# Kernel optimization log

Hardware: AMD Instinct MI355X
Metric: run time of the kernel (lower is better)

Reference implementation:

```python
import jax, jax.numpy as jnp
import numpy as np

N_NODES = 100000
N_EDGES = 1600000
D_FEAT = 128
HIDDEN = 128
N_CLASSES = 10
N_GRAPHS = 512


def setup_inputs() -> dict:
    key = jax.random.key(0)
    ks = jax.random.split(key, 8)
    x = jax.random.normal(ks[0], (N_NODES, D_FEAT), dtype=jnp.float32)
    edge_index = jax.random.randint(ks[1], (2, N_EDGES), 0, N_NODES, dtype=jnp.int64)
    batch = jnp.sort(jax.random.randint(ks[2], (N_NODES,), 0, N_GRAPHS, dtype=jnp.int64))
    s = 1.0 / np.sqrt(D_FEAT)
    W1 = jax.random.normal(ks[3], (D_FEAT, HIDDEN), dtype=jnp.float32) * s
    W2 = jax.random.normal(ks[4], (HIDDEN, HIDDEN), dtype=jnp.float32) * s
    W3 = jax.random.normal(ks[5], (HIDDEN, HIDDEN), dtype=jnp.float32) * s
    Wl = jax.random.normal(ks[6], (HIDDEN, N_CLASSES), dtype=jnp.float32) * s
    return {
        'x': x, 'edge_index': edge_index, 'batch': batch,
        'W1': W1, 'b1': jnp.zeros((HIDDEN,), jnp.float32),
        'W2': W2, 'b2': jnp.zeros((HIDDEN,), jnp.float32),
        'W3': W3, 'b3': jnp.zeros((HIDDEN,), jnp.float32),
        'Wl': Wl, 'bl': jnp.zeros((N_CLASSES,), jnp.float32),
    }


def _gcn_norm(edge_index, n_nodes):
    # add self-loops + symmetric normalization (PyG GCNConv defaults)
    loop = jnp.arange(n_nodes, dtype=edge_index.dtype)
    src = jnp.concatenate([edge_index[0], loop])
    dst = jnp.concatenate([edge_index[1], loop])
    deg = jax.ops.segment_sum(jnp.ones_like(dst, jnp.float32), dst, num_segments=n_nodes)
    dinv = jnp.where(deg > 0, jax.lax.rsqrt(deg), 0.0)
    norm = dinv[src] * dinv[dst]  # [E+N]
    return src, dst, norm


def _gcn_conv(x, src, dst, norm, W, b, n_nodes):
    h = x @ W                                   # [N, H]
    msg = norm[:, None] * h[src]                # gather + scale, [E+N, H]
    out = jax.ops.segment_sum(msg, dst, num_segments=n_nodes)  # scatter-add
    return out + b


def reference(x, edge_index, batch, W1, b1, W2, b2, W3, b3, Wl, bl):
    n = x.shape[0]
    src, dst, norm = _gcn_norm(edge_index, n)
    h = jax.nn.relu(_gcn_conv(x, src, dst, norm, W1, b1, n))
    h = jax.nn.relu(_gcn_conv(h, src, dst, norm, W2, b2, n))
    h = _gcn_conv(h, src, dst, norm, W3, b3, n)
    # global mean pool over graphs
    sums = jax.ops.segment_sum(h, batch, num_segments=N_GRAPHS)        # [G, H]
    cnts = jax.ops.segment_sum(jnp.ones((n,), jnp.float32), batch, num_segments=N_GRAPHS)
    pooled = sums / jnp.maximum(cnts, 1.0)[:, None]
    # dropout is identity in eval mode
    return pooled @ Wl + bl                                            # [G, C]
```

## Files before the change

### kernel.cpp

```cpp
#include <hip/hip_runtime.h>
#include <cstdint>
#include <cstddef>

typedef _Float16 half8 __attribute__((ext_vector_type(8)));
typedef float    f32x4 __attribute__((ext_vector_type(4)));

#define NBLK 512
#define BSHIFT 8

static __device__ __forceinline__ float4 ld4(const float* p) {
    return *reinterpret_cast<const float4*>(p);
}

static __device__ __forceinline__ void ld8h(const _Float16* p, float* f) {
    half8 v = *reinterpret_cast<const half8*>(p);
#pragma unroll
    for (int k = 0; k < 8; ++k) f[k] = (float)v[k];
}


__global__ __launch_bounds__(256)
void binA_count(const int* __restrict__ dst, int* __restrict__ cntM,
                int e, int nb, int tile) {
    __shared__ int lc[512];
    const int t = threadIdx.x, j = blockIdx.x;
    lc[t] = 0; lc[t + 256] = 0;
    __syncthreads();
    const int lo = j * tile;
    const int hi = min(e, lo + tile);
    for (int i = lo + t; i < hi; i += 256) atomicAdd(&lc[dst[i] >> BSHIFT], 1);
    __syncthreads();
    for (int b = t; b < nb; b += 256) cntM[b * NBLK + j] = lc[b];
}

__global__ __launch_bounds__(256)
void scan1_kernel(const int* __restrict__ cnt, int* __restrict__ blockSums, int n) {
    __shared__ int ts[256];
    const int t = threadIdx.x;
    const int base = blockIdx.x * 1024 + t * 4;
    int s = 0;
    if (base + 3 < n) {
        int4 q = *reinterpret_cast<const int4*>(cnt + base);
        s = q.x + q.y + q.z + q.w;
    } else {
#pragma unroll
        for (int j = 0; j < 4; ++j) if (base + j < n) s += cnt[base + j];
    }
    ts[t] = s;
    __syncthreads();
    for (int off = 128; off > 0; off >>= 1) {
        if (t < off) ts[t] += ts[t + off];
        __syncthreads();
    }
    if (t == 0) blockSums[blockIdx.x] = ts[0];
}

__global__ __launch_bounds__(1024)
void scan_top_kernel(const int* __restrict__ blockSums, int* __restrict__ blockOff,
                     int* __restrict__ total, int nb) {
    __shared__ int ls[1024];
    const int t = threadIdx.x;
    ls[t] = (t < nb) ? blockSums[t] : 0;
    __syncthreads();
    for (int off = 1; off < 1024; off <<= 1) {
        int v = (t >= off) ? ls[t - off] : 0;
        __syncthreads();
        ls[t] += v;
        __syncthreads();
    }
    if (t < nb) blockOff[t] = (t == 0) ? 0 : ls[t - 1];
    if (t == 1023) total[0] = ls[1023];
}

__global__ __launch_bounds__(256)
void scan2_kernel(const int* __restrict__ cnt, const int* __restrict__ blockOff,
                  int* __restrict__ outp, int n) {
    __shared__ int ts[256];
    const int t = threadIdx.x;
    const int base = blockIdx.x * 1024 + t * 4;
    int v[4] = {0, 0, 0, 0};
    if (base + 3 < n) {
        int4 q = *reinterpret_cast<const int4*>(cnt + base);
        v[0] = q.x; v[1] = q.y; v[2] = q.z; v[3] = q.w;
    } else {
#pragma unroll
        for (int j = 0; j < 4; ++j) if (base + j < n) v[j] = cnt[base + j];
    }
    int s = v[0] + v[1] + v[2] + v[3];
    ts[t] = s;
    __syncthreads();
    for (int off = 1; off < 256; off <<= 1) {
        int x = (t >= off) ? ts[t - off] : 0;
        __syncthreads();
        ts[t] += x;
        __syncthreads();
    }
    int excl = blockOff[blockIdx.x] + ((t == 0) ? 0 : ts[t - 1]);
#pragma unroll
    for (int j = 0; j < 4; ++j) {
        if (base + j < n) outp[base + j] = excl;
        excl += v[j];
    }
}

__global__ __launch_bounds__(256)
void binA_place(const int* __restrict__ src, const int* __restrict__ dst,
                const int* __restrict__ offM, int2* __restrict__ staging,
                int e, int nb, int tile) {
    __shared__ int cur[512];
    const int t = threadIdx.x, j = blockIdx.x;
    for (int b = t; b < nb; b += 256) cur[b] = offM[b * NBLK + j];
    __syncthreads();
    const int lo = j * tile;
    const int hi = min(e, lo + tile);
    for (int i = lo + t; i < hi; i += 256) {
        int s = src[i];
        int d = dst[i];
        int pos = atomicAdd(&cur[d >> BSHIFT], 1);
        staging[pos] = make_int2(s, d);
    }
}

__global__ __launch_bounds__(256)
void bucket_rows(const int2* __restrict__ staging, const int* __restrict__ offM,
                 int* __restrict__ rowptr, float* __restrict__ dinv,
                 int n, int nb, int e) {
    __shared__ int lc[256];
    __shared__ int ls[256];
    const int b = blockIdx.x, t = threadIdx.x;
    const int base = offM[b * NBLK];
    const int end  = (b + 1 < nb) ? offM[(b + 1) * NBLK] : e;
    const int d0 = b << BSHIFT;
    const int R  = min(n - d0, 256);
    lc[t] = 0;
    __syncthreads();
    for (int i = base + t; i < end; i += 256) atomicAdd(&lc[staging[i].y - d0], 1);
    __syncthreads();
    const int deg = lc[t];
    ls[t] = deg;
    __syncthreads();
    for (int off = 1; off < 256; off <<= 1) {
        int v = (t >= off) ? ls[t - off] : 0;
        __syncthreads();
        ls[t] += v;
        __syncthreads();
    }
    int excl = (t == 0) ? 0 : ls[t - 1];
    if (t < R) {
        rowptr[d0 + t] = base + excl;
        dinv[d0 + t]   = rsqrtf((float)(deg + 1));
    }
    if (b == nb - 1 && t == 0) rowptr[n] = e;
}

__global__ __launch_bounds__(256)
void bucket_scatter(const int2* __restrict__ staging, const int* __restrict__ offM,
                    const int* __restrict__ rowptr, const float* __restrict__ dinv,
                    int2* __restrict__ rec, int n, int nb, int e) {
    __shared__ int   cur[256];
    __shared__ float ldv[256];
    const int b = blockIdx.x, t = threadIdx.x;
    const int base = offM[b * NBLK];
    const int end  = (b + 1 < nb) ? offM[(b + 1) * NBLK] : e;
    const int d0 = b << BSHIFT;
    const int R  = min(n - d0, 256);
    if (t < R) {
        cur[t] = rowptr[d0 + t];
        ldv[t] = dinv[d0 + t];
    }
    __syncthreads();
    for (int i = base + t; i < end; i += 256) {
        int2 q = staging[i];
        int dl = q.y - d0;
        int pos = atomicAdd(&cur[dl], 1);
        float w = dinv[q.x] * ldv[dl];
        rec[pos] = make_int2(q.x, __float_as_int(w));
    }
}

template<int IN32>
__global__ __launch_bounds__(256)
void gemm_mfma_kernel(const void* __restrict__ Xv, const float* __restrict__ W,
                      _Float16* __restrict__ H16, int n) {
    __shared__ _Float16 Wt[128][136];
    __shared__ _Float16 Sw[4][16][136];

    const int t = threadIdx.x;
#pragma unroll
    for (int j = 0; j < 16; ++j) {
        int i4 = t + 256 * j;
        int k  = i4 >> 5;
        int c4 = (i4 & 31) * 4;
        float4 v = ld4(W + (size_t)i4 * 4);
        Wt[c4 + 0][k] = (_Float16)v.x;
        Wt[c4 + 1][k] = (_Float16)v.y;
        Wt[c4 + 2][k] = (_Float16)v.z;
        Wt[c4 + 3][k] = (_Float16)v.w;
    }
    __syncthreads();

    const int wave = t >> 6;
    const int l    = t & 63;
    const int lr   = l & 15;
    const int lk   = l >> 4;
    const int rowA = blockIdx.x * 64 + wave * 16 + lr;

    half8 a[4];
#pragma unroll
    for (int ks = 0; ks < 4; ++ks) {
#pragma unroll
        for (int j = 0; j < 8; ++j) a[ks][j] = (_Float16)0.f;
    }
    if (rowA < n) {
        if (IN32) {
            const float* X = (const float*)Xv;
#pragma unroll
            for (int ks = 0; ks < 4; ++ks) {
                const float* p = X + (size_t)rowA * 128 + ks * 32 + lk * 8;
                float4 f0 = ld4(p);
                float4 f1 = ld4(p + 4);
                a[ks][0] = (_Float16)f0.x; a[ks][1] = (_Float16)f0.y;
                a[ks][2] = (_Float16)f0.z; a[ks][3] = (_Float16)f0.w;
                a[ks][4] = (_Float16)f1.x; a[ks][5] = (_Float16)f1.y;
                a[ks][6] = (_Float16)f1.z; a[ks][7] = (_Float16)f1.w;
            }
        } else {
            const _Float16* X = (const _Float16*)Xv;
#pragma unroll
            for (int ks = 0; ks < 4; ++ks)
                a[ks] = *reinterpret_cast<const half8*>(X + (size_t)rowA * 128 + ks * 32 + lk * 8);
        }
    }

#pragma unroll
    for (int tt = 0; tt < 8; ++tt) {
        f32x4 acc = {0.f, 0.f, 0.f, 0.f};
#pragma unroll
        for (int ks = 0; ks < 4; ++ks) {
            half8 b = *reinterpret_cast<const half8*>(&Wt[tt * 16 + lr][ks * 32 + lk * 8]);
            acc = __builtin_amdgcn_mfma_f32_16x16x32_f16(a[ks], b, acc, 0, 0, 0);
        }
#pragma unroll
        for (int r = 0; r < 4; ++r)
            Sw[wave][lk * 4 + r][tt * 16 + lr] = (_Float16)acc[r];
    }
    __syncthreads();

#pragma unroll
    for (int j = 0; j < 4; ++j) {
        int chunk = l + 64 * j;
        int r  = chunk >> 4;
        int c8 = chunk & 15;
        int gr = blockIdx.x * 64 + wave * 16 + r;
        if (gr < n) {
            half8 v = *reinterpret_cast<const half8*>(&Sw[wave][r][c8 * 8]);
            *reinterpret_cast<half8*>(H16 + (size_t)gr * 128 + c8 * 8) = v;
        }
    }
}

template<int OUT16>
__global__ __launch_bounds__(256)
void gather_kernel(const int* __restrict__ rowptr, const int2* __restrict__ rec,
                   const float* __restrict__ dinv,
                   const _Float16* __restrict__ h16, const float* __restrict__ bias,
                   void* __restrict__ outb, int n, int do_relu) {
    int gid  = blockIdx.x * blockDim.x + threadIdx.x;
    int node = gid >> 4;
    int lane = gid & 15;
    if (node >= n) return;

    int rs = rowptr[node];
    int re = rowptr[node + 1];
    float di = dinv[node];
    const int fo = lane * 8;

    float acc[8];
    {
        float f[8];
        ld8h(h16 + (size_t)node * 128 + fo, f);
        float c = di * di;
#pragma unroll
        for (int k = 0; k < 8; ++k) acc[k] = c * f[k];
    }

    for (int e0 = rs; e0 < re; e0 += 16) {
        int m = re - e0;
        if (m > 16) m = 16;
        int   sI = 0;
        float wI = 0.f;
        if (lane < m) {
            int2 q = rec[e0 + lane];
            sI = q.x;
            wI = __int_as_float(q.y);
        }
        int j = 0;
        for (; j + 1 < m; j += 2) {
            int   s0 = __shfl(sI, j, 16);
            float w0 = __shfl(wI, j, 16);
            int   s1 = __shfl(sI, j + 1, 16);
            float w1 = __shfl(wI, j + 1, 16);
            float f0[8], f1[8];
            ld8h(h16 + (size_t)s0 * 128 + fo, f0);
            ld8h(h16 + (size_t)s1 * 128 + fo, f1);
#pragma unroll
            for (int k = 0; k < 8; ++k) {
                acc[k] = fmaf(w0, f0[k], acc[k]);
                acc[k] = fmaf(w1, f1[k], acc[k]);
            }
        }
        if (j < m) {
            int   s0 = __shfl(sI, j, 16);
            float w0 = __shfl(wI, j, 16);
            float f0[8];
            ld8h(h16 + (size_t)s0 * 128 + fo, f0);
#pragma unroll
            for (int k = 0; k < 8; ++k) acc[k] = fmaf(w0, f0[k], acc[k]);
        }
    }

    float4 b0 = ld4(bias + fo);
    float4 b1 = ld4(bias + fo + 4);
    acc[0] += b0.x; acc[1] += b0.y; acc[2] += b0.z; acc[3] += b0.w;
    acc[4] += b1.x; acc[5] += b1.y; acc[6] += b1.z; acc[7] += b1.w;
    if (do_relu) {
#pragma unroll
        for (int k = 0; k < 8; ++k) acc[k] = fmaxf(acc[k], 0.f);
    }
    if (OUT16) {
        half8 v;
#pragma unroll
        for (int k = 0; k < 8; ++k) v[k] = (_Float16)acc[k];
        *reinterpret_cast<half8*>((_Float16*)outb + (size_t)node * 128 + fo) = v;
    } else {
        float* op = (float*)outb + (size_t)node * 128 + fo;
        *reinterpret_cast<float4*>(op)     = make_float4(acc[0], acc[1], acc[2], acc[3]);
        *reinterpret_cast<float4*>(op + 4) = make_float4(acc[4], acc[5], acc[6], acc[7]);
    }
}

__global__ __launch_bounds__(256)
void pool_kernel(const _Float16* __restrict__ h, const int* __restrict__ batch,
                 float* __restrict__ pooled, int n) {
    __shared__ f32x4 red[16][34];
    int g = blockIdx.x;
    int lo = 0, hi = n;
    while (lo < hi) { int mid = (lo + hi) >> 1; if (batch[mid] < g) lo = mid + 1; else hi = mid; }
    int start = lo;
    hi = n;
    while (lo < hi) { int mid = (lo + hi) >> 1; if (batch[mid] < g + 1) lo = mid + 1; else hi = mid; }
    int end = lo;

    const int t   = threadIdx.x;
    const int grp = t >> 4;
    const int ln  = t & 15;

    float acc[8] = {0.f, 0.f, 0.f, 0.f, 0.f, 0.f, 0.f, 0.f};
    for (int i = start + grp; i < end; i += 16) {
        float f[8];
        ld8h(h + (size_t)i * 128 + ln * 8, f);
#pragma unroll
        for (int k = 0; k < 8; ++k) acc[k] += f[k];
    }
    red[grp][ln * 2]     = (f32x4){acc[0], acc[1], acc[2], acc[3]};
    red[grp][ln * 2 + 1] = (f32x4){acc[4], acc[5], acc[6], acc[7]};
    __syncthreads();
#pragma unroll
    for (int off = 8; off > 0; off >>= 1) {
        if (grp < off) {
            red[grp][ln * 2]     += red[grp + off][ln * 2];
            red[grp][ln * 2 + 1] += red[grp + off][ln * 2 + 1];
        }
        __syncthreads();
    }
    if (t < 128) {
        float cnt = (float)(end - start);
        pooled[g * 128 + t] = red[0][t >> 2][t & 3] / fmaxf(cnt, 1.0f);
    }
}

__global__ void final_kernel(const float* __restrict__ pooled, const float* __restrict__ Wl,
                             const float* __restrict__ bl, float* __restrict__ out, int n_classes) {
    __shared__ float ps[128];
    int g = blockIdx.x;
    int t = threadIdx.x;
    ps[t]      = pooled[g * 128 + t];
    ps[t + 64] = pooled[g * 128 + 64 + t];
    __syncthreads();
    if (t < n_classes) {
        float acc = bl[t];
        for (int k = 0; k < 128; ++k)
            acc = fmaf(ps[k], Wl[k * n_classes + t], acc);
        out[g * n_classes + t] = acc;
    }
}

extern "C" void kernel_launch(void* const* d_in, const int* in_sizes, int n_in,
                              void* d_out, int out_size, void* d_ws, size_t ws_size,
                              hipStream_t stream) {
    const float* x     = (const float*)d_in[0];
    const int*   ei    = (const int*)d_in[1];
    const int*   batch = (const int*)d_in[2];
    const float* W1 = (const float*)d_in[3];
    const float* b1 = (const float*)d_in[4];
    const float* W2 = (const float*)d_in[5];
    const float* b2 = (const float*)d_in[6];
    const float* W3 = (const float*)d_in[7];
    const float* b3 = (const float*)d_in[8];
    const float* Wl = (const float*)d_in[9];
    const float* bl = (const float*)d_in[10];
    float* out = (float*)d_out;

    const int N = in_sizes[0] / 128;
    const int E = in_sizes[1] / 2;
    const int C = 10;
    const int G = out_size / C;

    const int* srcI = ei;
    const int* dstI = ei + E;

    const int NB   = (N + 255) >> BSHIFT;
    const int M    = NB * NBLK;
    const int TILE = (E + NBLK - 1) / NBLK;
    const int scanB = (M + 1023) / 1024;

    char* w = (char*)d_ws;
    size_t off = 0;
    auto alloc = [&](size_t bytes) -> void* {
        void* p = w + off;
        off = (off + bytes + 255) & ~(size_t)255;
        return p;
    };

    int*      rowptr    = (int*)alloc((size_t)(N + 1) * 4);
    float*    dinv      = (float*)alloc((size_t)N * 4);
    int2*     rec       = (int2*)alloc((size_t)E * 8);
    int2*     staging   = (int2*)alloc((size_t)E * 8);
    int*      cntM      = (int*)alloc((size_t)M * 4);
    int*      offM      = (int*)alloc((size_t)M * 4);
    int*      blockSums = (int*)alloc((size_t)scanB * 4);
    int*      blockOff  = (int*)alloc((size_t)scanB * 4);
    int*      scrTotal  = (int*)alloc(256);
    _Float16* h16       = (_Float16*)alloc((size_t)N * 128 * 2);
    _Float16* act16     = (_Float16*)alloc((size_t)N * 128 * 2);
    float*    pooled    = (float*)alloc((size_t)G * 128 * 4);

    binA_count<<<NBLK, 256, 0, stream>>>(dstI, cntM, E, NB, TILE);
    scan1_kernel<<<scanB, 256, 0, stream>>>(cntM, blockSums, M);
    scan_top_kernel<<<1, 1024, 0, stream>>>(blockSums, blockOff, scrTotal, scanB);
    scan2_kernel<<<scanB, 256, 0, stream>>>(cntM, blockOff, offM, M);
    binA_place<<<NBLK, 256, 0, stream>>>(srcI, dstI, offM, staging, E, NB, TILE);
    bucket_rows<<<NB, 256, 0, stream>>>(staging, offM, rowptr, dinv, N, NB, E);
    bucket_scatter<<<NB, 256, 0, stream>>>(staging, offM, rowptr, dinv, rec, N, NB, E);

    const int gemmBlocks = (N + 63) / 64;
    const int gathBlocks = (N * 16 + 255) / 256;

    gemm_mfma_kernel<1><<<gemmBlocks, 256, 0, stream>>>(x, W1, h16, N);
    gather_kernel<1><<<gathBlocks, 256, 0, stream>>>(rowptr, rec, dinv, h16, b1, act16, N, 1);
    gemm_mfma_kernel<0><<<gemmBlocks, 256, 0, stream>>>(act16, W2, h16, N);
    gather_kernel<1><<<gathBlocks, 256, 0, stream>>>(rowptr, rec, dinv, h16, b2, act16, N, 1);
    gemm_mfma_kernel<0><<<gemmBlocks, 256, 0, stream>>>(act16, W3, h16, N);
    gather_kernel<1><<<gathBlocks, 256, 0, stream>>>(rowptr, rec, dinv, h16, b3, act16, N, 0);

    pool_kernel<<<G, 256, 0, stream>>>(act16, batch, pooled, N);
    final_kernel<<<G, 64, 0, stream>>>(pooled, Wl, bl, out, C);
}
```

Measured before the change: 361.7 us.

## Store hidden features in feature-sliced layout to localize gather working set

Hidden activations change from row-major [N,128] to eight feature slices of [N,16]. The gather kernel now handles one slice per block, with two threads per node each reading 16-byte chunks. This is meant to make each slice's working set (about 3.2MB) fit in cache so random neighbor gathers hit cache more often. In exchange, the edge records are re-read eight times, once per slice, and each thread loops over the node's edges serially instead of sharing them across lanes with shuffles. The GEMM and pool kernels are changed to read and write the new layout, and the edge loads and output store use nontemporal hints.

Result: slower. 746.3 us (+106.3%).

```diff
diff --git a/kernel.cpp b/kernel.cpp
--- a/kernel.cpp
+++ b/kernel.cpp
@@ -7,6 +7,7 @@
 
 #define NBLK 512
 #define BSHIFT 8
+#define NSLICE 8
 
 static __device__ __forceinline__ float4 ld4(const float* p) {
     return *reinterpret_cast<const float4*>(p);
@@ -227,8 +228,11 @@
         } else {
             const _Float16* X = (const _Float16*)Xv;
 #pragma unroll
-            for (int ks = 0; ks < 4; ++ks)
-                a[ks] = *reinterpret_cast<const half8*>(X + (size_t)rowA * 128 + ks * 32 + lk * 8);
+            for (int ks = 0; ks < 4; ++ks) {
+                int sl = ks * 2 + (lk >> 1);
+                a[ks] = *reinterpret_cast<const half8*>(
+                    X + ((size_t)sl * n + rowA) * 16 + (lk & 1) * 8);
+            }
         }
     }
 
@@ -254,89 +258,79 @@
         int gr = blockIdx.x * 64 + wave * 16 + r;
         if (gr < n) {
             half8 v = *reinterpret_cast<const half8*>(&Sw[wave][r][c8 * 8]);
-            *reinterpret_cast<half8*>(H16 + (size_t)gr * 128 + c8 * 8) = v;
+            *reinterpret_cast<half8*>(
+                H16 + ((size_t)(c8 >> 1) * n + gr) * 16 + (c8 & 1) * 8) = v;
         }
     }
 }
 
-template<int OUT16>
 __global__ __launch_bounds__(256)
 void gather_kernel(const int* __restrict__ rowptr, const int2* __restrict__ rec,
                    const float* __restrict__ dinv,
                    const _Float16* __restrict__ h16, const float* __restrict__ bias,
-                   void* __restrict__ outb, int n, int do_relu) {
-    int gid  = blockIdx.x * blockDim.x + threadIdx.x;
-    int node = gid >> 4;
-    int lane = gid & 15;
+                   _Float16* __restrict__ outb, int n, int do_relu) {
+    const int slice = blockIdx.x & 7;
+    const int tile  = blockIdx.x >> 3;
+    const int t     = threadIdx.x;
+    const int node  = tile * 128 + (t >> 1);
+    const int po    = (t & 1) * 8;
     if (node >= n) return;
+
+    const size_t sb = (size_t)slice * n;
 
     int rs = rowptr[node];
     int re = rowptr[node + 1];
     float di = dinv[node];
-    const int fo = lane * 8;
 
     float acc[8];
     {
         float f[8];
-        ld8h(h16 + (size_t)node * 128 + fo, f);
+        ld8h(h16 + (sb + node) * 16 + po, f);
         float c = di * di;
 #pragma unroll
         for (int k = 0; k < 8; ++k) acc[k] = c * f[k];
     }
 
-    for (int e0 = rs; e0 < re; e0 += 16) {
-        int m = re - e0;
-        if (m > 16) m = 16;
-        int   sI = 0;
-        float wI = 0.f;
-        if (lane < m) {
-            int2 q = rec[e0 + lane];
-            sI = q.x;
-            wI = __int_as_float(q.y);
+    const unsigned long long* rp = (const unsigned long long*)rec;
+    int e0 = rs;
+    for (; e0 + 1 < re; e0 += 2) {
+        unsigned long long q0 = __builtin_nontemporal_load(rp + e0);
+        unsigned long long q1 = __builtin_nontemporal_load(rp + e0 + 1);
+        int   s0 = (int)(unsigned)(q0 & 0xffffffffull);
+        float w0 = __int_as_float((int)(unsigned)(q0 >> 32));
+        int   s1 = (int)(unsigned)(q1 & 0xffffffffull);
+        float w1 = __int_as_float((int)(unsigned)(q1 >> 32));
+        float f0[8], f1[8];
+        ld8h(h16 + (sb + s0) * 16 + po, f0);
+        ld8h(h16 + (sb + s1) * 16 + po, f1);
+#pragma unroll
+        for (int k = 0; k < 8; ++k) {
+            acc[k] = fmaf(w0, f0[k], acc[k]);
+            acc[k] = fmaf(w1, f1[k], acc[k]);
         }
-        int j = 0;
-        for (; j + 1 < m; j += 2) {
-            int   s0 = __shfl(sI, j, 16);
-            float w0 = __shfl(wI, j, 16);
-            int   s1 = __shfl(sI, j + 1, 16);
-            float w1 = __shfl(wI, j + 1, 16);
-            float f0[8], f1[8];
-            ld8h(h16 + (size_t)s0 * 128 + fo, f0);
-            ld8h(h16 + (size_t)s1 * 128 + fo, f1);
-#pragma unroll
-            for (int k = 0; k < 8; ++k) {
-                acc[k] = fmaf(w0, f0[k], acc[k]);
-                acc[k] = fmaf(w1, f1[k], acc[k]);
-            }
-        }
-        if (j < m) {
-            int   s0 = __shfl(sI, j, 16);
-            float w0 = __shfl(wI, j, 16);
-            float f0[8];
-            ld8h(h16 + (size_t)s0 * 128 + fo, f0);
-#pragma unroll
-            for (int k = 0; k < 8; ++k) acc[k] = fmaf(w0, f0[k], acc[k]);
-        }
-    }
-
-    float4 b0 = ld4(bias + fo);
-    float4 b1 = ld4(bias + fo + 4);
+    }
+    if (e0 < re) {
+        unsigned long long q0 = __builtin_nontemporal_load(rp + e0);
+        int   s0 = (int)(unsigned)(q0 & 0xffffffffull);
+        float w0 = __int_as_float((int)(unsigned)(q0 >> 32));
+        float f0[8];
+        ld8h(h16 + (sb + s0) * 16 + po, f0);
+#pragma unroll
+        for (int k = 0; k < 8; ++k) acc[k] = fmaf(w0, f0[k], acc[k]);
+    }
+
+    float4 b0 = ld4(bias + slice * 16 + po);
+    float4 b1 = ld4(bias + slice * 16 + po + 4);
     acc[0] += b0.x; acc[1] += b0.y; acc[2] += b0.z; acc[3] += b0.w;
     acc[4] += b1.x; acc[5] += b1.y; acc[6] += b1.z; acc[7] += b1.w;
     if (do_relu) {
 #pragma unroll
         for (int k = 0; k < 8; ++k) acc[k] = fmaxf(acc[k], 0.f);
     }
-    if (OUT16) {
-        half8 v;
-#pragma unroll
-        for (int k = 0; k < 8; ++k) v[k] = (_Float16)acc[k];
-        *reinterpret_cast<half8*>((_Float16*)outb + (size_t)node * 128 + fo) = v;
-    } else {
-        float* op = (float*)outb + (size_t)node * 128 + fo;
-        *reinterpret_cast<float4*>(op)     = make_float4(acc[0], acc[1], acc[2], acc[3]);
-        *reinterpret_cast<float4*>(op + 4) = make_float4(acc[4], acc[5], acc[6], acc[7]);
-    }
+    half8 v;
+#pragma unroll
+    for (int k = 0; k < 8; ++k) v[k] = (_Float16)acc[k];
+    __builtin_nontemporal_store(v, reinterpret_cast<half8*>(outb + (sb + node) * 16 + po));
 }
 
 __global__ __launch_bounds__(256)
@@ -358,7 +352,7 @@
     float acc[8] = {0.f, 0.f, 0.f, 0.f, 0.f, 0.f, 0.f, 0.f};
     for (int i = start + grp; i < end; i += 16) {
         float f[8];
-        ld8h(h + (size_t)i * 128 + ln * 8, f);
+        ld8h(h + ((size_t)(ln >> 1) * n + i) * 16 + (ln & 1) * 8, f);
 #pragma unroll
         for (int k = 0; k < 8; ++k) acc[k] += f[k];
     }
@@ -454,14 +448,14 @@
     bucket_scatter<<<NB, 256, 0, stream>>>(staging, offM, rowptr, dinv, rec, N, NB, E);
 
     const int gemmBlocks = (N + 63) / 64;
-    const int gathBlocks = (N * 16 + 255) / 256;
+    const int gathBlocks = ((N + 127) / 128) * NSLICE;
 
     gemm_mfma_kernel<1><<<gemmBlocks, 256, 0, stream>>>(x, W1, h16, N);
-    gather_kernel<1><<<gathBlocks, 256, 0, stream>>>(rowptr, rec, dinv, h16, b1, act16, N, 1);
+    gather_kernel<<<gathBlocks, 256, 0, stream>>>(rowptr, rec, dinv, h16, b1, act16, N, 1);
     gemm_mfma_kernel<0><<<gemmBlocks, 256, 0, stream>>>(act16, W2, h16, N);
-    gather_kernel<1><<<gathBlocks, 256, 0, stream>>>(rowptr, rec, dinv, h16, b2, act16, N, 1);
+    gather_kernel<<<gathBlocks, 256, 0, stream>>>(rowptr, rec, dinv, h16, b2, act16, N, 1);
     gemm_mfma_kernel<0><<<gemmBlocks, 256, 0, stream>>>(act16, W3, h16, N);
-    gather_kernel<1><<<gathBlocks, 256, 0, stream>>>(rowptr, rec, dinv, h16, b3, act16, N, 0);
+    gather_kernel<<<gathBlocks, 256, 0, stream>>>(rowptr, rec, dinv, h16, b3, act16, N, 0);
 
     pool_kernel<<<G, 256, 0, stream>>>(act16, batch, pooled, N);
     final_kernel<<<G, 64, 0, stream>>>(pooled, Wl, bl, out, C);
```
